# Performance work log

Hardware: AMD Instinct MI355X
Metric: run time of the kernel (lower is better)

## Reference

```python
import jax, jax.numpy as jnp
import numpy as np

B, C, CK, CV, W, H = 8, 256, 256, 256, 64, 64
EPS = 1e-6

def setup_inputs() -> dict:
    key = jax.random.key(0)
    ks = jax.random.split(key, 13)
    def wmat(k, shape, fan_in):
        return jax.random.normal(k, shape, jnp.float32) / np.float32(np.sqrt(fan_in))
    return {
        "x": jax.random.normal(ks[0], (B, C, W, H), jnp.float32),
        "qw": wmat(ks[1], (CK, C), C), "qb": jnp.zeros((CK,), jnp.float32),
        "kw": wmat(ks[2], (CK, C), C), "kb": jnp.zeros((CK,), jnp.float32),
        "vw": wmat(ks[3], (CV, C), C), "vb": jnp.zeros((CV,), jnp.float32),
        "rw": wmat(ks[4], (C, CV), CV), "rb": jnp.zeros((C,), jnp.float32),
        "c1w": wmat(ks[5], (C, C, 3, 3), C * 9), "c1b": jnp.zeros((C,), jnp.float32),
        "c2w": wmat(ks[6], (C, C, 3, 3), C * 9), "c2b": jnp.zeros((C,), jnp.float32),
    }

def reference(x, qw, qb, kw, kb, vw, vb, rw, rb, c1w, c1b, c2w, c2b):
    Bz, Cc, Wd, Hd = x.shape
    n = Wd * Hd
    xf = x.reshape(Bz, Cc, n)                                  # [b,c,n]
    Q = jnp.einsum('oc,bcn->bon', qw, xf) + qb[None, :, None]  # 1x1 conv
    K = jnp.einsum('oc,bcn->bon', kw, xf) + kb[None, :, None]
    V = jnp.einsum('oc,bcn->bon', vw, xf) + vb[None, :, None]
    # l2 norm over channel dim (per token), exactly as torch.norm(dim=-2)
    Qn = Q / jnp.linalg.norm(Q, axis=1, keepdims=True)
    Kn = K / jnp.linalg.norm(K, axis=1, keepdims=True)
    Qt = jnp.transpose(Qn, (0, 2, 1))                          # [b,n,ck]
    # head loops in the original sum over the full channel dim -> single einsum
    agg_dom = jnp.einsum('bnk,bk->bn', Qt, Kn.sum(-1))         # [b,n]
    denom = 1.0 / (n + agg_dom + EPS)                          # [b,n]
    vsum = V.sum(-1)                                           # [b,cv]
    kv = jnp.einsum('bkn,bcn->bkc', Kn, V)                     # K^T V, [b,ck,cv]
    qkv = jnp.einsum('bnk,bkc->bcn', Qt, kv)                   # [b,cv,n]
    wv = (vsum[:, :, None] + qkv) * denom[:, None, :]
    wv = wv.reshape(Bz, -1, Hd, Wd)                            # matches torch .view(b,cv,h,w)
    attn = jnp.einsum('oc,bchw->bohw', rw, wv) + rb[None, :, None, None]
    dn = ('NCHW', 'OIHW', 'NCHW')
    h = jax.lax.conv_general_dilated(attn, c1w, (1, 1), 'SAME', dimension_numbers=dn) + c1b[None, :, None, None]
    h = jax.lax.conv_general_dilated(h, c2w, (1, 1), 'SAME', dimension_numbers=dn) + c2b[None, :, None, None]
    return h * x + x
```

## Files before the change

kernel.cpp:

```cpp
#include <hip/hip_runtime.h>
#include <math.h>


typedef unsigned short u16;
typedef __attribute__((ext_vector_type(8))) short short8;
typedef __attribute__((ext_vector_type(4))) float f32x4;
typedef __attribute__((ext_vector_type(4))) unsigned short us4v;

#define ASYNC16(g, l) __builtin_amdgcn_global_load_lds( \
    (const __attribute__((address_space(1))) unsigned int*)(g), \
    (__attribute__((address_space(3))) unsigned int*)(l), 16, 0, 0)

static __device__ __forceinline__ float b2f(u16 h) {
  unsigned int u = ((unsigned int)h) << 16;
  return __builtin_bit_cast(float, u);
}
static __device__ __forceinline__ u16 f2b(float f) {
  unsigned int u = __builtin_bit_cast(unsigned int, f);
  u += 0x7fffu + ((u >> 16) & 1u);
  return (u16)(u >> 16);
}

#define NB 1048576L

__global__ __launch_bounds__(256) void prep1(
    const float* __restrict__ qw, const float* __restrict__ kw,
    const float* __restrict__ vw, const float* __restrict__ rw,
    const float* __restrict__ c1w, const float* __restrict__ c2w,
    const float* __restrict__ kb, const float* __restrict__ vb,
    const float* __restrict__ rb,
    u16* __restrict__ qw16, u16* __restrict__ kvw16, u16* __restrict__ rwT16,
    u16* __restrict__ wr1, u16* __restrict__ wr2,
    float* __restrict__ kvbias, float* __restrict__ zbuf, float* __restrict__ T)
{
  if (blockIdx.x >= 5633) {
    int m = blockIdx.x - 5633, co = threadIdx.x;
    float r = rb[co];
    const float* p = c1w + (long)m * 2304 + co * 9;
    float lv[9];
#pragma unroll
    for (int d = 0; d < 9; d++) lv[d] = p[d] * r;
#pragma unroll
    for (int d = 0; d < 9; d++)
#pragma unroll
      for (int off = 32; off; off >>= 1) lv[d] += __shfl_down(lv[d], off, 64);
    __shared__ float red[4][9];
    int w = co >> 6, l = co & 63;
    if (l == 0)
#pragma unroll
      for (int d = 0; d < 9; d++) red[w][d] = lv[d];
    __syncthreads();
    if (co < 9) T[m * 9 + co] = red[0][co] + red[1][co] + red[2][co] + red[3][co];
    return;
  }
  if (blockIdx.x == 5632) {
    int t = threadIdx.x;
    if (t < 256) { kvbias[t] = kb[t]; kvbias[t + 256] = vb[t]; }
    if (t < 64) zbuf[t] = 0.f;
    return;
  }
  long g = (long)blockIdx.x * 256 + threadIdx.x;
  if (g < 65536) {
    qw16[g] = f2b(qw[g]);
  } else if (g < 196608) {
    long e = g - 65536;
    kvw16[e] = f2b(e < 65536 ? kw[e] : vw[e - 65536]);
  } else if (g < 262144) {
    long e = g - 196608;
    int cv = e >> 8, co = e & 255;
    rwT16[e] = f2b(rw[co * 256 + cv]);
  } else if (g < 851968) {
    long e = g - 262144;
    int m = e / 2304, r = e - m * 2304;
    int d = r >> 8, c = r & 255;
    wr1[e] = f2b(c1w[m * 2304 + c * 9 + d]);
  } else {
    long e = g - 851968;
    int m = e / 2304, r = e - m * 2304;
    int d = r >> 8, c = r & 255;
    wr2[e] = f2b(c2w[m * 2304 + c * 9 + d]);
  }
}

__global__ __launch_bounds__(256) void corr_transX(
    const float* __restrict__ T, const float* __restrict__ c1b,
    float* __restrict__ corr,
    const float* __restrict__ x, u16* __restrict__ xT)
{
  __shared__ float Tl[64][65];
  int bb = blockIdx.x, t = threadIdx.x;
  if (bb < 4096) {
    int e = bb * 256 + t;
    int m = e & 255, p = e >> 8;
    int y = p >> 6, xx = p & 63;
    float s = c1b[m];
#pragma unroll
    for (int d = 0; d < 9; d++) {
      int dy = d / 3 - 1, dx = d - (d / 3) * 3 - 1;
      if ((unsigned)(y + dy) < 64u && (unsigned)(xx + dx) < 64u) s += T[m * 9 + d];
    }
    corr[e] = s;
    return;
  }
  int lin = bb - 4096;
  int n0 = (lin & 63) * 64, c0 = ((lin >> 6) & 3) * 64, b = lin >> 8;
#pragma unroll
  for (int i = 0; i < 4; i++) {
    int c = (t >> 4) + i * 16, nn = (t & 15) * 4;
    float4 v = *(const float4*)&x[(long)b * NB + (long)(c0 + c) * 4096 + n0 + nn];
    Tl[c][nn] = v.x; Tl[c][nn + 1] = v.y; Tl[c][nn + 2] = v.z; Tl[c][nn + 3] = v.w;
  }
  __syncthreads();
#pragma unroll
  for (int i = 0; i < 4; i++) {
    int n = (t >> 4) + i * 16, cc = (t & 15) * 4;
    us4v o;
#pragma unroll
    for (int e = 0; e < 4; e++) o[e] = f2b(Tl[cc + e][n]);
    *(us4v*)&xT[(long)b * NB + (long)(n0 + n) * 256 + c0 + cc] = o;
  }
}

__global__ __launch_bounds__(256) void gemm3(
    const u16* __restrict__ wr1, const u16* __restrict__ rwT16, u16* __restrict__ w1p,
    const u16* __restrict__ xT, const u16* __restrict__ qw16, u16* __restrict__ Qt,
    const u16* __restrict__ kvw16, u16* __restrict__ KV,
    const float* __restrict__ qb, const float* __restrict__ kvbias)
{
  __shared__ __align__(16) u16 As[2][128 * 32];
  __shared__ __align__(16) u16 Bs[2][128 * 32];
  int lin = blockIdx.x;
  const u16 *A, *B;
  u16* out;
  const float *p1, *p2;
  long i0, j0, aoff, boff, ooff, sR;
  if (lin < 36) {
    int bx = lin & 1, by = lin >> 1;
    A = wr1; B = rwT16; out = w1p;
    i0 = by * 128; j0 = bx * 128;
    aoff = 0; boff = 0; ooff = 0; sR = 256;
    p1 = nullptr; p2 = nullptr;
  } else if (lin < 548) {
    int e = lin - 36;
    int bx = e & 1, by = (e >> 1) & 31, b = e >> 6;
    A = xT; B = qw16; out = Qt;
    i0 = by * 128; j0 = bx * 128;
    aoff = (long)b * NB; boff = 0; ooff = (long)b * NB; sR = 256;
    p1 = nullptr; p2 = qb;
  } else {
    int e = lin - 548;
    int bx = e & 31, by = (e >> 5) & 3, b = e >> 7;
    A = kvw16; B = xT; out = KV;
    i0 = by * 128; j0 = bx * 128;
    aoff = 0; boff = (long)b * NB; ooff = (long)b * 2 * NB; sR = 4096;
    p1 = kvbias; p2 = nullptr;
  }
  const u16* Ab = A + aoff + i0 * 256;
  const u16* Bb = B + boff + j0 * 256;
  int t = threadIdx.x, wave = t >> 6, lane = t & 63;
  int wi = (wave >> 1) * 64, wj = (wave & 1) * 64;
  int li = lane & 15, quad = lane >> 4;
  int qs = (lane & 3) ^ ((lane >> 3) & 3);
  int qx = quad ^ ((lane >> 1) & 3);
  int r0 = (wave * 128 + lane) >> 2;
  int r1 = (wave * 128 + 64 + lane) >> 2;
  f32x4 acc[4][4];
#pragma unroll
  for (int i = 0; i < 4; i++)
#pragma unroll
    for (int j = 0; j < 4; j++) acc[i][j] = (f32x4){0.f, 0.f, 0.f, 0.f};

  auto STAGE = [&](int kc, int buf) {
    int k0 = kc * 32;
    ASYNC16(Ab + (long)r0 * 256 + k0 + qs * 8, &As[buf][(wave * 128) * 8]);
    ASYNC16(Bb + (long)r0 * 256 + k0 + qs * 8, &Bs[buf][(wave * 128) * 8]);
    ASYNC16(Ab + (long)r1 * 256 + k0 + qs * 8, &As[buf][(wave * 128 + 64) * 8]);
    ASYNC16(Bb + (long)r1 * 256 + k0 + qs * 8, &Bs[buf][(wave * 128 + 64) * 8]);
  };

  int cur = 0;
  STAGE(0, 0);
#pragma unroll 1
  for (int kc = 0; kc < 8; kc++) {
    if (kc + 1 < 8) {
      STAGE(kc + 1, cur ^ 1);
      asm volatile("s_waitcnt vmcnt(4)" ::: "memory");
    } else {
      asm volatile("s_waitcnt vmcnt(0)" ::: "memory");
    }
    __builtin_amdgcn_s_barrier();
    const u16* as = &As[cur][0];
    const u16* bs = &Bs[cur][0];
    short8 af[4], bf[4];
#pragma unroll
    for (int s = 0; s < 4; s++) af[s] = *(const short8*)&as[(wi + s * 16 + li) * 32 + qx * 8];
#pragma unroll
    for (int s = 0; s < 4; s++) bf[s] = *(const short8*)&bs[(wj + s * 16 + li) * 32 + qx * 8];
#pragma unroll
    for (int si = 0; si < 4; si++)
#pragma unroll
      for (int sj = 0; sj < 4; sj++)
        acc[si][sj] = __builtin_amdgcn_mfma_f32_16x16x32_bf16(af[si], bf[sj], acc[si][sj], 0, 0, 0);
    __builtin_amdgcn_s_barrier();
    cur ^= 1;
  }

#pragma unroll
  for (int si = 0; si < 4; si++)
#pragma unroll
    for (int sj = 0; sj < 4; sj++) {
      long col = j0 + wj + sj * 16 + li;
#pragma unroll
      for (int r = 0; r < 4; r++) {
        long row = i0 + wi + si * 16 + quad * 4 + r;
        float v = acc[si][sj][r];
        if (p1) v += p1[row];
        if (p2) v += p2[col];
        out[ooff + row * sR + col] = f2b(v);
      }
    }
}

__global__ __launch_bounds__(256) void gemm_nt(
    const u16* __restrict__ A, const u16* __restrict__ B, u16* __restrict__ out,
    int K, int lda, int ldb, long sAb, long sBb, long sOb, long sR, long sC,
    int mode, const float* __restrict__ p1, const float* __restrict__ p2,
    const float* __restrict__ p3)
{
  __shared__ __align__(16) u16 As[2][128 * 64];
  __shared__ __align__(16) u16 Bs[2][128 * 64];
  int b = blockIdx.z;
  long i0 = (long)blockIdx.y * 128;
  long j0 = (long)blockIdx.x * 128;
  const u16* Ab = A + b * sAb + i0 * lda;
  const u16* Bb = B + b * sBb + j0 * ldb;
  int t = threadIdx.x, wave = t >> 6, lane = t & 63;
  int wi = (wave >> 1) * 64, wj = (wave & 1) * 64;
  int li = lane & 15, quad = lane >> 4;
  int qs8 = (lane & 7) ^ ((lane >> 3) & 7);
  f32x4 acc[4][4];
#pragma unroll
  for (int i = 0; i < 4; i++)
#pragma unroll
    for (int j = 0; j < 4; j++) acc[i][j] = (f32x4){0.f, 0.f, 0.f, 0.f};

  auto STAGE = [&](int kc, int buf) {
    long k0 = (long)kc * 64 + qs8 * 8;
#pragma unroll
    for (int j = 0; j < 4; j++) {
      int row = (wave * 4 + j) * 8 + (lane >> 3);
      ASYNC16(Ab + (long)row * lda + k0, &As[buf][(wave * 4 + j) * 512]);
      ASYNC16(Bb + (long)row * ldb + k0, &Bs[buf][(wave * 4 + j) * 512]);
    }
  };

  int nk = K >> 6, cur = 0;
  STAGE(0, 0);
#pragma unroll 1
  for (int kc = 0; kc < nk; kc++) {
    if (kc + 1 < nk) {
      STAGE(kc + 1, cur ^ 1);
      asm volatile("s_waitcnt vmcnt(8)" ::: "memory");
    } else {
      asm volatile("s_waitcnt vmcnt(0)" ::: "memory");
    }
    __builtin_amdgcn_s_barrier();
    const u16* as = &As[cur][0];
    const u16* bs = &Bs[cur][0];
#pragma unroll
    for (int kk = 0; kk < 2; kk++) {
      short8 af[4], bf[4];
      int slot = (((kk << 2) | quad) ^ (li & 7)) * 8;
#pragma unroll
      for (int s = 0; s < 4; s++) af[s] = *(const short8*)&as[(wi + s * 16 + li) * 64 + slot];
#pragma unroll
      for (int s = 0; s < 4; s++) bf[s] = *(const short8*)&bs[(wj + s * 16 + li) * 64 + slot];
#pragma unroll
      for (int si = 0; si < 4; si++)
#pragma unroll
        for (int sj = 0; sj < 4; sj++)
          acc[si][sj] = __builtin_amdgcn_mfma_f32_16x16x32_bf16(af[si], bf[sj], acc[si][sj], 0, 0, 0);
    }
    __builtin_amdgcn_s_barrier();
    cur ^= 1;
  }

#pragma unroll
  for (int si = 0; si < 4; si++)
#pragma unroll
    for (int sj = 0; sj < 4; sj++) {
      long col = j0 + wj + sj * 16 + li;
#pragma unroll
      for (int r = 0; r < 4; r++) {
        long row = i0 + wi + si * 16 + quad * 4 + r;
        float v = acc[si][sj][r];
        if (mode == 0) {
          if (p1) v += p1[row];
          if (p2) v += p2[col];
        } else {
          v = (v * p3[b * 4096 + row] + p1[b * 256 + col]) * p2[b * 4096 + row];
        }
        out[b * sOb + row * sR + col * sC] = f2b(v);
      }
    }
}

__global__ __launch_bounds__(256) void gemm_kv(
    const u16* __restrict__ KV, float* __restrict__ part)
{
  __shared__ __align__(16) u16 As[2][128 * 64];
  __shared__ __align__(16) u16 Bs[2][128 * 64];
  int z = blockIdx.z;
  int b = z & 7, sp = z >> 3;
  long i0 = (long)blockIdx.y * 128;
  long j0 = (long)blockIdx.x * 128;
  const u16* Ab = KV + (long)b * 2 * NB + i0 * 4096;
  const u16* Bb = KV + (long)b * 2 * NB + NB + j0 * 4096;
  int t = threadIdx.x, wave = t >> 6, lane = t & 63;
  int wi = (wave >> 1) * 64, wj = (wave & 1) * 64;
  int li = lane & 15, quad = lane >> 4;
  int qs8 = (lane & 7) ^ ((lane >> 3) & 7);
  f32x4 acc[4][4];
#pragma unroll
  for (int i = 0; i < 4; i++)
#pragma unroll
    for (int j = 0; j < 4; j++) acc[i][j] = (f32x4){0.f, 0.f, 0.f, 0.f};

  auto STAGE = [&](int kc, int buf) {
    long k0 = (long)sp * 512 + kc * 64 + qs8 * 8;
#pragma unroll
    for (int j = 0; j < 4; j++) {
      int row = (wave * 4 + j) * 8 + (lane >> 3);
      ASYNC16(Ab + (long)row * 4096 + k0, &As[buf][(wave * 4 + j) * 512]);
      ASYNC16(Bb + (long)row * 4096 + k0, &Bs[buf][(wave * 4 + j) * 512]);
    }
  };

  int cur = 0;
  STAGE(0, 0);
#pragma unroll 1
  for (int kc = 0; kc < 8; kc++) {
    if (kc + 1 < 8) {
      STAGE(kc + 1, cur ^ 1);
      asm volatile("s_waitcnt vmcnt(8)" ::: "memory");
    } else {
      asm volatile("s_waitcnt vmcnt(0)" ::: "memory");
    }
    __builtin_amdgcn_s_barrier();
    const u16* as = &As[cur][0];
    const u16* bs = &Bs[cur][0];
#pragma unroll
    for (int kk = 0; kk < 2; kk++) {
      short8 af[4], bf[4];
      int slot = (((kk << 2) | quad) ^ (li & 7)) * 8;
#pragma unroll
      for (int s = 0; s < 4; s++) af[s] = *(const short8*)&as[(wi + s * 16 + li) * 64 + slot];
#pragma unroll
      for (int s = 0; s < 4; s++) bf[s] = *(const short8*)&bs[(wj + s * 16 + li) * 64 + slot];
#pragma unroll
      for (int si = 0; si < 4; si++)
#pragma unroll
        for (int sj = 0; sj < 4; sj++)
          acc[si][sj] = __builtin_amdgcn_mfma_f32_16x16x32_bf16(af[si], bf[sj], acc[si][sj], 0, 0, 0);
    }
    __builtin_amdgcn_s_barrier();
    cur ^= 1;
  }

  float* outp = part + ((long)sp * 8 + b) * 65536;
#pragma unroll
  for (int si = 0; si < 4; si++)
#pragma unroll
    for (int sj = 0; sj < 4; sj++) {
      long col = j0 + wj + sj * 16 + li;
#pragma unroll
      for (int r = 0; r < 4; r++) {
        long row = i0 + wi + si * 16 + quad * 4 + r;
        outp[col * 256 + row] = acc[si][sj][r];
      }
    }
}

__global__ __launch_bounds__(256) void redkv_qden(
    const float* __restrict__ part, u16* __restrict__ kvT,
    const u16* __restrict__ Qt, const float* __restrict__ ksum,
    float* __restrict__ rq, float* __restrict__ den)
{
  int bb = blockIdx.x;
  if (bb < 2048) {
    int g = bb * 256 + threadIdx.x;
    float s = 0.f;
#pragma unroll
    for (int sp = 0; sp < 8; sp++) s += part[(long)sp * 524288 + g];
    kvT[g] = f2b(s);
    return;
  }
  int row = (bb - 2048) * 4 + (threadIdx.x >> 6);
  int lane = threadIdx.x & 63;
  int b = row >> 12;
  us4v v = *(const us4v*)(Qt + (long)row * 256 + lane * 4);
  float4 ks = *(const float4*)&ksum[b * 256 + lane * 4];
  float f0 = b2f(v[0]), f1 = b2f(v[1]), f2 = b2f(v[2]), f3 = b2f(v[3]);
  float s = f0 * f0 + f1 * f1 + f2 * f2 + f3 * f3;
  float s2 = f0 * ks.x + f1 * ks.y + f2 * ks.z + f3 * ks.w;
#pragma unroll
  for (int m = 32; m; m >>= 1) {
    s += __shfl_xor(s, m, 64);
    s2 += __shfl_xor(s2, m, 64);
  }
  if (lane == 0) {
    float r = 1.0f / sqrtf(s);
    rq[row] = r;
    den[row] = 1.0f / (4096.0f + s2 * r + 1e-6f);
  }
}

__global__ __launch_bounds__(256) void sumsqK(
    const u16* __restrict__ KV, float* __restrict__ rsqK)
{
  __shared__ float red[16][68];
  int b = blockIdx.x >> 6, nc = blockIdx.x & 63;
  int n0 = nc * 64;
  int t = threadIdx.x;
  int nn = (t & 15) * 4, cg = t >> 4;
  const u16* base = KV + (long)b * 2 * NB;
  float s0 = 0.f, s1 = 0.f, s2 = 0.f, s3 = 0.f;
  for (int st = 0; st < 16; st++) {
    int c = cg + st * 16;
    us4v v = *(const us4v*)(base + (long)c * 4096 + n0 + nn);
    float a = b2f(v[0]), bb = b2f(v[1]), cc = b2f(v[2]), dd = b2f(v[3]);
    s0 = fmaf(a, a, s0); s1 = fmaf(bb, bb, s1);
    s2 = fmaf(cc, cc, s2); s3 = fmaf(dd, dd, s3);
  }
  red[cg][nn] = s0; red[cg][nn + 1] = s1; red[cg][nn + 2] = s2; red[cg][nn + 3] = s3;
  __syncthreads();
  if (t < 64) {
    float s = 0.f;
#pragma unroll
    for (int g = 0; g < 16; g++) s += red[g][t];
    rsqK[b * 4096 + n0 + t] = 1.0f / sqrtf(s);
  }
}

__global__ __launch_bounds__(256) void scale_sums(
    u16* __restrict__ KV, const float* __restrict__ rsqK,
    float* __restrict__ ksum, float* __restrict__ vsum)
{
  int z = blockIdx.x;
  int isV = z >> 11, rem = z & 2047, b = rem >> 8, c = rem & 255;
  u16* row = KV + (long)b * 2 * NB + (long)isV * NB + (long)c * 4096;
  const float* rq = rsqK + b * 4096;
  int t = threadIdx.x;
  float s = 0.f;
  short8 v0 = *(const short8*)&row[t * 16];
  short8 v1 = *(const short8*)&row[t * 16 + 8];
  if (!isV) {
    short8 o0, o1;
#pragma unroll
    for (int e = 0; e < 8; e++) {
      float a = b2f((u16)v0[e]) * rq[t * 16 + e];
      float bb = b2f((u16)v1[e]) * rq[t * 16 + 8 + e];
      s += a + bb;
      o0[e] = (short)f2b(a); o1[e] = (short)f2b(bb);
    }
    *(short8*)&row[t * 16] = o0;
    *(short8*)&row[t * 16 + 8] = o1;
  } else {
#pragma unroll
    for (int e = 0; e < 8; e++) s += b2f((u16)v0[e]) + b2f((u16)v1[e]);
  }
#pragma unroll
  for (int off = 32; off; off >>= 1) s += __shfl_down(s, off, 64);
  __shared__ float red[4];
  if ((t & 63) == 0) red[t >> 6] = s;
  __syncthreads();
  if (t == 0)
    (isV ? vsum : ksum)[b * 256 + c] = red[0] + red[1] + red[2] + red[3];
}

__global__ __launch_bounds__(512, 2) void conv_gemm(
    const u16* __restrict__ inT, const u16* __restrict__ wr,
    const float* __restrict__ cb, const float* __restrict__ xres,
    const float* __restrict__ zbuf,
    u16* __restrict__ out16, float* __restrict__ out32, int mode)
{
  __shared__ __align__(16) u16 S[2 * 24576];

  int lin = blockIdx.x;
  int b   = lin & 7;
  int n0  = (lin >> 3) * 128;

  int t = threadIdx.x, wave = t >> 6, lane = t & 63;
  int wm = (wave >> 1) * 64, wn = (wave & 1) * 64;
  int li = lane & 15, quad = lane >> 4;
  int qs8 = (lane & 7) ^ ((lane >> 3) & 7);
  const u16* inb = inT + (long)b * NB;

  int rr = wave * 8 + (lane >> 3);
  const u16* Ap0 = wr + (long)(rr)       * 2304 + qs8 * 8;
  const u16* Ap1 = wr + (long)(rr + 64)  * 2304 + qs8 * 8;
  const u16* Ap2 = wr + (long)(rr + 128) * 2304 + qs8 * 8;
  const u16* Ap3 = wr + (long)(rr + 192) * 2304 + qs8 * 8;
  const u16* Bp0 = inb + (long)(n0 + rr) * 256 + qs8 * 8;
  const u16* Bp1 = inb + (long)(n0 + 64 + rr) * 256 + qs8 * 8;
  const u16* zp  = (const u16*)zbuf + qs8 * 8;
  int yb0 = n0 >> 6, xb = rr;

  f32x4 acc[4][4];
#pragma unroll
  for (int i = 0; i < 4; i++)
#pragma unroll
    for (int j = 0; j < 4; j++) acc[i][j] = (f32x4){0.f, 0.f, 0.f, 0.f};

  auto STAGE = [&](int ks, int buf) {
    int d = ks >> 2;
    int dy = d / 3 - 1, dx = d - (d / 3) * 3 - 1;
    long shA = (long)ks * 64;
    long shB = (long)(dy * 64 + dx) * 256 + (ks & 3) * 64;
    u16* base = &S[buf * 24576];
    ASYNC16(Ap0 + shA, base + wave * 512);
    ASYNC16(Ap1 + shA, base + 4096 + wave * 512);
    ASYNC16(Ap2 + shA, base + 8192 + wave * 512);
    ASYNC16(Ap3 + shA, base + 12288 + wave * 512);
    bool v0 = ((unsigned)(yb0 + dy) < 64u) && ((unsigned)(xb + dx) < 64u);
    bool v1 = ((unsigned)(yb0 + 1 + dy) < 64u) && ((unsigned)(xb + dx) < 64u);
    ASYNC16(v0 ? Bp0 + shB : zp, base + 16384 + wave * 512);
    ASYNC16(v1 ? Bp1 + shB : zp, base + 20480 + wave * 512);
  };

  int cur = 0;
  STAGE(0, 0);
#pragma unroll 1
  for (int ks = 0; ks < 36; ks++) {
    if (ks + 1 < 36) {
      STAGE(ks + 1, cur ^ 1);
      asm volatile("s_waitcnt vmcnt(6)" ::: "memory");
    } else {
      asm volatile("s_waitcnt vmcnt(0)" ::: "memory");
    }
    __builtin_amdgcn_s_barrier();
    const u16* as = &S[cur * 24576];
    const u16* bs = as + 16384;
#pragma unroll
    for (int kk = 0; kk < 2; kk++) {
      short8 af[4], bf[4];
      int slot = (((kk << 2) | quad) ^ (lane & 7)) * 8;
#pragma unroll
      for (int s = 0; s < 4; s++) af[s] = *(const short8*)&as[(wm + s * 16 + li) * 64 + slot];
#pragma unroll
      for (int s = 0; s < 4; s++) bf[s] = *(const short8*)&bs[(wn + s * 16 + li) * 64 + slot];
#pragma unroll
      for (int si = 0; si < 4; si++)
#pragma unroll
        for (int sj = 0; sj < 4; sj++)
          acc[si][sj] = __builtin_amdgcn_mfma_f32_16x16x32_bf16(af[si], bf[sj], acc[si][sj], 0, 0, 0);
    }
    __builtin_amdgcn_s_barrier();
    cur ^= 1;
  }

#pragma unroll
  for (int si = 0; si < 4; si++)
#pragma unroll
    for (int sj = 0; sj < 4; sj++) {
      int n = n0 + wn + sj * 16 + li;
      int m0 = wm + si * 16 + quad * 4;
      if (mode == 0) {
        f32x4 c4 = *(const f32x4*)&cb[(long)n * 256 + m0];
        us4v o;
#pragma unroll
        for (int r = 0; r < 4; r++) o[r] = f2b(acc[si][sj][r] + c4[r]);
        *(us4v*)&out16[(long)b * NB + (long)n * 256 + m0] = o;
      } else {
#pragma unroll
        for (int r = 0; r < 4; r++) {
          int m = m0 + r;
          float v = acc[si][sj][r] + cb[m];
          long a = (long)b * NB + (long)m * 4096 + n;
          float xv = xres[a];
          out32[a] = fmaf(v, xv, xv);
        }
      }
    }
}

extern "C" void kernel_launch(void* const* d_in, const int* in_sizes, int n_in,
                              void* d_out, int out_size, void* d_ws, size_t ws_size,
                              hipStream_t stream)
{
  const float* x   = (const float*)d_in[0];
  const float* qw  = (const float*)d_in[1];
  const float* qb  = (const float*)d_in[2];
  const float* kw  = (const float*)d_in[3];
  const float* kb  = (const float*)d_in[4];
  const float* vw  = (const float*)d_in[5];
  const float* vb  = (const float*)d_in[6];
  const float* rw  = (const float*)d_in[7];
  const float* rb  = (const float*)d_in[8];
  const float* c1w = (const float*)d_in[9];
  const float* c1b = (const float*)d_in[10];
  const float* c2w = (const float*)d_in[11];
  const float* c2b = (const float*)d_in[12];

  u16* U     = (u16*)d_ws;
  u16* xT16  = U;
  u16* Qt16  = U + 8388608;
  u16* KV16  = U + 16777216;
  u16* wr2   = U + 33554432;
  u16* kvT16 = U + 34144256;
  float* Fws = (float*)(U + 34668544);
  float* ksum = Fws;
  float* vsum = Fws + 2048;
  float* zbuf = Fws + 4096;

  char* ob = (char*)d_out;
  float* kvpart = (float*)(ob + 0);
  float* den    = (float*)(ob + 16777216);
  float* rsqK   = (float*)(ob + 16908288);
  float* corr   = (float*)(ob + 17039360);
  u16*   w1p16  = (u16*)(ob + 21233664);
  u16*   wr1    = (u16*)(ob + 22413312);
  float* T      = (float*)(ob + 23592960);
  u16*   rwT16  = (u16*)(ob + 23629824);
  u16*   qw16   = (u16*)(ob + 23760896);
  u16*   kvw16  = (u16*)(ob + 23891968);
  float* kvbias = (float*)(ob + 24154112);
  float* rq     = (float*)(ob + 24158208);
  float* outF   = (float*)d_out;

  u16* wvT16 = xT16;
  u16* h1T16 = Qt16;

  dim3 blk(256);

  prep1<<<5889, blk, 0, stream>>>(qw, kw, vw, rw, c1w, c2w, kb, vb, rb,
                                  qw16, kvw16, rwT16, wr1, wr2, kvbias, zbuf, T);
  corr_transX<<<6144, blk, 0, stream>>>(T, c1b, corr, x, xT16);

  gemm3<<<1572, blk, 0, stream>>>(wr1, rwT16, w1p16, xT16, qw16, Qt16,
                                  kvw16, KV16, qb, kvbias);

  sumsqK<<<512, blk, 0, stream>>>(KV16, rsqK);
  scale_sums<<<4096, blk, 0, stream>>>(KV16, rsqK, ksum, vsum);

  gemm_kv<<<dim3(2, 2, 64), blk, 0, stream>>>(KV16, kvpart);
  redkv_qden<<<10240, blk, 0, stream>>>(kvpart, kvT16, Qt16, ksum, rq, den);

  gemm_nt<<<dim3(2, 32, 8), blk, 0, stream>>>(Qt16, kvT16, wvT16,
      256, 256, 256, NB, 65536L, NB, 256L, 1L, 2, vsum, den, rq);

  conv_gemm<<<256, 512, 0, stream>>>(wvT16, w1p16, corr, nullptr, zbuf,
                                     h1T16, nullptr, 0);
  conv_gemm<<<256, 512, 0, stream>>>(h1T16, wr2, c2b, x, zbuf,
                                     nullptr, outF, 1);
}
```

Baseline: 320.1 us.

## Move corr fill into gemm3, specialize wv GEMM, shrink gemm_kv tiles

The corr bias-map computation moves out of the transpose kernel and becomes extra tail blocks of gemm3, so the transpose kernel now only transposes x. The generic gemm_nt used for the Q·KV product is replaced by gemm_wv, a dedicated kernel with K-chunks of 32, a different LDS swizzle and a hardcoded epilogue. gemm_kv moves from 128x128 to 64x128 tiles, doubling its block count (256 to 512) to fill more CUs. The trade-offs are more per-tile overhead and synchronisation in exchange for better occupancy, plus gemm3 blocks whose work is now uneven.

New measurement: 309.3 us. 1.03x faster.

```diff
diff --git a/kernel.cpp b/kernel.cpp
--- a/kernel.cpp
+++ b/kernel.cpp
@@ -82,27 +82,11 @@
   }
 }
 
-__global__ __launch_bounds__(256) void corr_transX(
-    const float* __restrict__ T, const float* __restrict__ c1b,
-    float* __restrict__ corr,
+__global__ __launch_bounds__(256) void transX(
     const float* __restrict__ x, u16* __restrict__ xT)
 {
   __shared__ float Tl[64][65];
-  int bb = blockIdx.x, t = threadIdx.x;
-  if (bb < 4096) {
-    int e = bb * 256 + t;
-    int m = e & 255, p = e >> 8;
-    int y = p >> 6, xx = p & 63;
-    float s = c1b[m];
-#pragma unroll
-    for (int d = 0; d < 9; d++) {
-      int dy = d / 3 - 1, dx = d - (d / 3) * 3 - 1;
-      if ((unsigned)(y + dy) < 64u && (unsigned)(xx + dx) < 64u) s += T[m * 9 + d];
-    }
-    corr[e] = s;
-    return;
-  }
-  int lin = bb - 4096;
+  int lin = blockIdx.x, t = threadIdx.x;
   int n0 = (lin & 63) * 64, c0 = ((lin >> 6) & 3) * 64, b = lin >> 8;
 #pragma unroll
   for (int i = 0; i < 4; i++) {
@@ -125,11 +109,26 @@
     const u16* __restrict__ wr1, const u16* __restrict__ rwT16, u16* __restrict__ w1p,
     const u16* __restrict__ xT, const u16* __restrict__ qw16, u16* __restrict__ Qt,
     const u16* __restrict__ kvw16, u16* __restrict__ KV,
-    const float* __restrict__ qb, const float* __restrict__ kvbias)
+    const float* __restrict__ qb, const float* __restrict__ kvbias,
+    const float* __restrict__ T, const float* __restrict__ c1b,
+    float* __restrict__ corr)
 {
   __shared__ __align__(16) u16 As[2][128 * 32];
   __shared__ __align__(16) u16 Bs[2][128 * 32];
   int lin = blockIdx.x;
+  if (lin >= 1572) {
+    int e = (lin - 1572) * 256 + threadIdx.x;
+    int m = e & 255, p = e >> 8;
+    int y = p >> 6, xx = p & 63;
+    float s = c1b[m];
+#pragma unroll
+    for (int d = 0; d < 9; d++) {
+      int dy = d / 3 - 1, dx = d - (d / 3) * 3 - 1;
+      if ((unsigned)(y + dy) < 64u && (unsigned)(xx + dx) < 64u) s += T[m * 9 + d];
+    }
+    corr[e] = s;
+    return;
+  }
   const u16 *A, *B;
   u16* out;
   const float *p1, *p2;
@@ -221,23 +220,26 @@
     }
 }
 
-__global__ __launch_bounds__(256) void gemm_nt(
-    const u16* __restrict__ A, const u16* __restrict__ B, u16* __restrict__ out,
-    int K, int lda, int ldb, long sAb, long sBb, long sOb, long sR, long sC,
-    int mode, const float* __restrict__ p1, const float* __restrict__ p2,
-    const float* __restrict__ p3)
-{
-  __shared__ __align__(16) u16 As[2][128 * 64];
-  __shared__ __align__(16) u16 Bs[2][128 * 64];
-  int b = blockIdx.z;
-  long i0 = (long)blockIdx.y * 128;
-  long j0 = (long)blockIdx.x * 128;
-  const u16* Ab = A + b * sAb + i0 * lda;
-  const u16* Bb = B + b * sBb + j0 * ldb;
+__global__ __launch_bounds__(256) void gemm_wv(
+    const u16* __restrict__ Qt, const u16* __restrict__ kvT, u16* __restrict__ wvT,
+    const float* __restrict__ vsum, const float* __restrict__ den,
+    const float* __restrict__ rq)
+{
+  __shared__ __align__(16) u16 As[2][128 * 32];
+  __shared__ __align__(16) u16 Bs[2][128 * 32];
+  int lin = blockIdx.x;
+  int bx = lin & 1, by = (lin >> 1) & 31, b = lin >> 6;
+  long i0 = (long)by * 128;
+  long j0 = (long)bx * 128;
+  const u16* Ab = Qt + (long)b * NB + i0 * 256;
+  const u16* Bb = kvT + (long)b * 65536 + j0 * 256;
   int t = threadIdx.x, wave = t >> 6, lane = t & 63;
   int wi = (wave >> 1) * 64, wj = (wave & 1) * 64;
   int li = lane & 15, quad = lane >> 4;
-  int qs8 = (lane & 7) ^ ((lane >> 3) & 7);
+  int qs = (lane & 3) ^ ((lane >> 3) & 3);
+  int qx = quad ^ ((lane >> 1) & 3);
+  int r0 = (wave * 128 + lane) >> 2;
+  int r1 = (wave * 128 + 64 + lane) >> 2;
   f32x4 acc[4][4];
 #pragma unroll
   for (int i = 0; i < 4; i++)
@@ -245,95 +247,11 @@
     for (int j = 0; j < 4; j++) acc[i][j] = (f32x4){0.f, 0.f, 0.f, 0.f};
 
   auto STAGE = [&](int kc, int buf) {
-    long k0 = (long)kc * 64 + qs8 * 8;
-#pragma unroll
-    for (int j = 0; j < 4; j++) {
-      int row = (wave * 4 + j) * 8 + (lane >> 3);
-      ASYNC16(Ab + (long)row * lda + k0, &As[buf][(wave * 4 + j) * 512]);
-      ASYNC16(Bb + (long)row * ldb + k0, &Bs[buf][(wave * 4 + j) * 512]);
-    }
-  };
-
-  int nk = K >> 6, cur = 0;
-  STAGE(0, 0);
-#pragma unroll 1
-  for (int kc = 0; kc < nk; kc++) {
-    if (kc + 1 < nk) {
-      STAGE(kc + 1, cur ^ 1);
-      asm volatile("s_waitcnt vmcnt(8)" ::: "memory");
-    } else {
-      asm volatile("s_waitcnt vmcnt(0)" ::: "memory");
-    }
-    __builtin_amdgcn_s_barrier();
-    const u16* as = &As[cur][0];
-    const u16* bs = &Bs[cur][0];
-#pragma unroll
-    for (int kk = 0; kk < 2; kk++) {
-      short8 af[4], bf[4];
-      int slot = (((kk << 2) | quad) ^ (li & 7)) * 8;
-#pragma unroll
-      for (int s = 0; s < 4; s++) af[s] = *(const short8*)&as[(wi + s * 16 + li) * 64 + slot];
-#pragma unroll
-      for (int s = 0; s < 4; s++) bf[s] = *(const short8*)&bs[(wj + s * 16 + li) * 64 + slot];
-#pragma unroll
-      for (int si = 0; si < 4; si++)
-#pragma unroll
-        for (int sj = 0; sj < 4; sj++)
-          acc[si][sj] = __builtin_amdgcn_mfma_f32_16x16x32_bf16(af[si], bf[sj], acc[si][sj], 0, 0, 0);
-    }
-    __builtin_amdgcn_s_barrier();
-    cur ^= 1;
-  }
-
-#pragma unroll
-  for (int si = 0; si < 4; si++)
-#pragma unroll
-    for (int sj = 0; sj < 4; sj++) {
-      long col = j0 + wj + sj * 16 + li;
-#pragma unroll
-      for (int r = 0; r < 4; r++) {
-        long row = i0 + wi + si * 16 + quad * 4 + r;
-        float v = acc[si][sj][r];
-        if (mode == 0) {
-          if (p1) v += p1[row];
-          if (p2) v += p2[col];
-        } else {
-          v = (v * p3[b * 4096 + row] + p1[b * 256 + col]) * p2[b * 4096 + row];
-        }
-        out[b * sOb + row * sR + col * sC] = f2b(v);
-      }
-    }
-}
-
-__global__ __launch_bounds__(256) void gemm_kv(
-    const u16* __restrict__ KV, float* __restrict__ part)
-{
-  __shared__ __align__(16) u16 As[2][128 * 64];
-  __shared__ __align__(16) u16 Bs[2][128 * 64];
-  int z = blockIdx.z;
-  int b = z & 7, sp = z >> 3;
-  long i0 = (long)blockIdx.y * 128;
-  long j0 = (long)blockIdx.x * 128;
-  const u16* Ab = KV + (long)b * 2 * NB + i0 * 4096;
-  const u16* Bb = KV + (long)b * 2 * NB + NB + j0 * 4096;
-  int t = threadIdx.x, wave = t >> 6, lane = t & 63;
-  int wi = (wave >> 1) * 64, wj = (wave & 1) * 64;
-  int li = lane & 15, quad = lane >> 4;
-  int qs8 = (lane & 7) ^ ((lane >> 3) & 7);
-  f32x4 acc[4][4];
-#pragma unroll
-  for (int i = 0; i < 4; i++)
-#pragma unroll
-    for (int j = 0; j < 4; j++) acc[i][j] = (f32x4){0.f, 0.f, 0.f, 0.f};
-
-  auto STAGE = [&](int kc, int buf) {
-    long k0 = (long)sp * 512 + kc * 64 + qs8 * 8;
-#pragma unroll
-    for (int j = 0; j < 4; j++) {
-      int row = (wave * 4 + j) * 8 + (lane >> 3);
-      ASYNC16(Ab + (long)row * 4096 + k0, &As[buf][(wave * 4 + j) * 512]);
-      ASYNC16(Bb + (long)row * 4096 + k0, &Bs[buf][(wave * 4 + j) * 512]);
-    }
+    int k0 = kc * 32;
+    ASYNC16(Ab + (long)r0 * 256 + k0 + qs * 8, &As[buf][(wave * 128) * 8]);
+    ASYNC16(Bb + (long)r0 * 256 + k0 + qs * 8, &Bs[buf][(wave * 128) * 8]);
+    ASYNC16(Ab + (long)r1 * 256 + k0 + qs * 8, &As[buf][(wave * 128 + 64) * 8]);
+    ASYNC16(Bb + (long)r1 * 256 + k0 + qs * 8, &Bs[buf][(wave * 128 + 64) * 8]);
   };
 
   int cur = 0;
@@ -342,23 +260,99 @@
   for (int kc = 0; kc < 8; kc++) {
     if (kc + 1 < 8) {
       STAGE(kc + 1, cur ^ 1);
-      asm volatile("s_waitcnt vmcnt(8)" ::: "memory");
+      asm volatile("s_waitcnt vmcnt(4)" ::: "memory");
     } else {
       asm volatile("s_waitcnt vmcnt(0)" ::: "memory");
     }
     __builtin_amdgcn_s_barrier();
     const u16* as = &As[cur][0];
     const u16* bs = &Bs[cur][0];
+    short8 af[4], bf[4];
+#pragma unroll
+    for (int s = 0; s < 4; s++) af[s] = *(const short8*)&as[(wi + s * 16 + li) * 32 + qx * 8];
+#pragma unroll
+    for (int s = 0; s < 4; s++) bf[s] = *(const short8*)&bs[(wj + s * 16 + li) * 32 + qx * 8];
+#pragma unroll
+    for (int si = 0; si < 4; si++)
+#pragma unroll
+      for (int sj = 0; sj < 4; sj++)
+        acc[si][sj] = __builtin_amdgcn_mfma_f32_16x16x32_bf16(af[si], bf[sj], acc[si][sj], 0, 0, 0);
+    __builtin_amdgcn_s_barrier();
+    cur ^= 1;
+  }
+
+#pragma unroll
+  for (int si = 0; si < 4; si++)
+#pragma unroll
+    for (int sj = 0; sj < 4; sj++) {
+      long col = j0 + wj + sj * 16 + li;
+#pragma unroll
+      for (int r = 0; r < 4; r++) {
+        long row = i0 + wi + si * 16 + quad * 4 + r;
+        float v = (acc[si][sj][r] * rq[b * 4096 + row] + vsum[b * 256 + col])
+                  * den[b * 4096 + row];
+        wvT[(long)b * NB + row * 256 + col] = f2b(v);
+      }
+    }
+}
+
+__global__ __launch_bounds__(256) void gemm_kv(
+    const u16* __restrict__ KV, float* __restrict__ part)
+{
+  __shared__ __align__(16) u16 As[2][64 * 64];
+  __shared__ __align__(16) u16 Bs[2][128 * 64];
+  int z = blockIdx.z;
+  int b = z & 7, sp = z >> 3;
+  long i0 = (long)blockIdx.y * 64;
+  long j0 = (long)blockIdx.x * 128;
+  const u16* Ab = KV + (long)b * 2 * NB + i0 * 4096;
+  const u16* Bb = KV + (long)b * 2 * NB + NB + j0 * 4096;
+  int t = threadIdx.x, wave = t >> 6, lane = t & 63;
+  int wm = (wave >> 1) * 32, wn = (wave & 1) * 64;
+  int li = lane & 15, quad = lane >> 4;
+  int qs8 = (lane & 7) ^ ((lane >> 3) & 7);
+  int rr = wave * 8 + (lane >> 3);
+  f32x4 acc[2][4];
+#pragma unroll
+  for (int i = 0; i < 2; i++)
+#pragma unroll
+    for (int j = 0; j < 4; j++) acc[i][j] = (f32x4){0.f, 0.f, 0.f, 0.f};
+
+  auto STAGE = [&](int kc, int buf) {
+    long k0 = (long)sp * 512 + kc * 64 + qs8 * 8;
+    u16* ab = &As[buf][0];
+    u16* bb = &Bs[buf][0];
+    ASYNC16(Ab + (long)(rr)      * 4096 + k0, ab + wave * 512);
+    ASYNC16(Ab + (long)(rr + 32) * 4096 + k0, ab + 2048 + wave * 512);
+    ASYNC16(Bb + (long)(rr)      * 4096 + k0, bb + wave * 512);
+    ASYNC16(Bb + (long)(rr + 32) * 4096 + k0, bb + 2048 + wave * 512);
+    ASYNC16(Bb + (long)(rr + 64) * 4096 + k0, bb + 4096 + wave * 512);
+    ASYNC16(Bb + (long)(rr + 96) * 4096 + k0, bb + 6144 + wave * 512);
+  };
+
+  int cur = 0;
+  STAGE(0, 0);
+#pragma unroll 1
+  for (int kc = 0; kc < 8; kc++) {
+    if (kc + 1 < 8) {
+      STAGE(kc + 1, cur ^ 1);
+      asm volatile("s_waitcnt vmcnt(6)" ::: "memory");
+    } else {
+      asm volatile("s_waitcnt vmcnt(0)" ::: "memory");
+    }
+    __builtin_amdgcn_s_barrier();
+    const u16* as = &As[cur][0];
+    const u16* bs = &Bs[cur][0];
 #pragma unroll
     for (int kk = 0; kk < 2; kk++) {
-      short8 af[4], bf[4];
-      int slot = (((kk << 2) | quad) ^ (li & 7)) * 8;
-#pragma unroll
-      for (int s = 0; s < 4; s++) af[s] = *(const short8*)&as[(wi + s * 16 + li) * 64 + slot];
-#pragma unroll
-      for (int s = 0; s < 4; s++) bf[s] = *(const short8*)&bs[(wj + s * 16 + li) * 64 + slot];
-#pragma unroll
-      for (int si = 0; si < 4; si++)
+      short8 af[2], bf[4];
+      int slot = (((kk << 2) | quad) ^ (lane & 7)) * 8;
+#pragma unroll
+      for (int s = 0; s < 2; s++) af[s] = *(const short8*)&as[(wm + s * 16 + li) * 64 + slot];
+#pragma unroll
+      for (int s = 0; s < 4; s++) bf[s] = *(const short8*)&bs[(wn + s * 16 + li) * 64 + slot];
+#pragma unroll
+      for (int si = 0; si < 2; si++)
 #pragma unroll
         for (int sj = 0; sj < 4; sj++)
           acc[si][sj] = __builtin_amdgcn_mfma_f32_16x16x32_bf16(af[si], bf[sj], acc[si][sj], 0, 0, 0);
@@ -369,13 +363,13 @@
 
   float* outp = part + ((long)sp * 8 + b) * 65536;
 #pragma unroll
-  for (int si = 0; si < 4; si++)
+  for (int si = 0; si < 2; si++)
 #pragma unroll
     for (int sj = 0; sj < 4; sj++) {
-      long col = j0 + wj + sj * 16 + li;
+      long col = j0 + wn + sj * 16 + li;
 #pragma unroll
       for (int r = 0; r < 4; r++) {
-        long row = i0 + wi + si * 16 + quad * 4 + r;
+        long row = i0 + wm + si * 16 + quad * 4 + r;
         outp[col * 256 + row] = acc[si][sj][r];
       }
     }
@@ -635,19 +629,18 @@
 
   prep1<<<5889, blk, 0, stream>>>(qw, kw, vw, rw, c1w, c2w, kb, vb, rb,
                                   qw16, kvw16, rwT16, wr1, wr2, kvbias, zbuf, T);
-  corr_transX<<<6144, blk, 0, stream>>>(T, c1b, corr, x, xT16);
-
-  gemm3<<<1572, blk, 0, stream>>>(wr1, rwT16, w1p16, xT16, qw16, Qt16,
-                                  kvw16, KV16, qb, kvbias);
+  transX<<<2048, blk, 0, stream>>>(x, xT16);
+
+  gemm3<<<5668, blk, 0, stream>>>(wr1, rwT16, w1p16, xT16, qw16, Qt16,
+                                  kvw16, KV16, qb, kvbias, T, c1b, corr);
 
   sumsqK<<<512, blk, 0, stream>>>(KV16, rsqK);
   scale_sums<<<4096, blk, 0, stream>>>(KV16, rsqK, ksum, vsum);
 
-  gemm_kv<<<dim3(2, 2, 64), blk, 0, stream>>>(KV16, kvpart);
+  gemm_kv<<<dim3(2, 4, 64), blk, 0, stream>>>(KV16, kvpart);
   redkv_qden<<<10240, blk, 0, stream>>>(kvpart, kvT16, Qt16, ksum, rq, den);
 
-  gemm_nt<<<dim3(2, 32, 8), blk, 0, stream>>>(Qt16, kvT16, wvT16,
-      256, 256, 256, NB, 65536L, NB, 256L, 1L, 2, vsum, den, rq);
+  gemm_wv<<<512, blk, 0, stream>>>(Qt16, kvT16, wvT16, vsum, den, rq);
 
   conv_gemm<<<256, 512, 0, stream>>>(wvT16, w1p16, corr, nullptr, zbuf,
                                      h1T16, nullptr, 0);
```
